# Optimization experiments

Hardware: AMD Instinct MI355X
Metric: run time of the kernel (lower is better)

The kernel has to match this reference:

```python
import jax, jax.numpy as jnp
import numpy as np

ALPHA = 0.2  # LeakyReLU negative slope


def setup_inputs() -> dict:
    key = jax.random.key(0)
    k1, k2, k3, k4 = jax.random.split(key, 4)
    B, T, D_in, H, S = 32, 1024, 64, 64, 2
    embedding = jax.random.normal(k1, (B, T, D_in), dtype=jnp.float32)
    x = jax.random.normal(k2, (S * B, T, D_in), dtype=jnp.float32)
    # xavier_uniform-ish scale for params
    W = jax.random.normal(k3, (D_in, H), dtype=jnp.float32) * (1.414 * np.sqrt(2.0 / (D_in + H)))
    a = jax.random.normal(k4, (2 * H, 1), dtype=jnp.float32) * (1.414 * np.sqrt(2.0 / (2 * H + 1)))
    return {"embedding": embedding, "x": x, "W": W, "a": a, "input_size": S}


def reference(embedding, x, W, a, input_size):
    # embedding: [B, T, D_in], W: [D_in, H], a: [2H, 1], x: [S*B, T, D_in]
    H = W.shape[1]
    h = jnp.einsum("btd,dh->bth", embedding, W)          # [B, T, H]
    a1 = a[:H, 0]                                        # attends to h_i (query side)
    a2 = a[H:, 0]                                        # attends to h_j (key side)
    f1 = h @ a1                                          # [B, T]
    f2 = h @ a2                                          # [B, T]
    # e_ij = leakyrelu(a1.h_i + a2.h_j) -- avoids materializing [B,T,T,2H]
    e = jax.nn.leaky_relu(f1[:, :, None] + f2[:, None, :], negative_slope=ALPHA)  # [B, T, T]
    attn = jax.nn.softmax(e, axis=2)                     # [B, T, T]
    attn_tiled = jnp.tile(attn, (input_size, 1, 1))      # [S*B, T, T] (dropout: eval mode, identity)
    out = jnp.einsum("bij,bjd->bid", attn_tiled, x)      # [S*B, T, D_in]
    return out
```

## Files before the change

kernel.cpp:

```cpp
#include <hip/hip_runtime.h>

typedef float  f32x4 __attribute__((ext_vector_type(4)));
typedef _Float16 h16x8 __attribute__((ext_vector_type(8)));
typedef _Float16 h16x2 __attribute__((ext_vector_type(2)));

#define LOG2E 1.4426950408889634f
#define ALPHA 0.2f

__device__ __forceinline__ float fexp2(float v) {
#if __has_builtin(__builtin_amdgcn_exp2f)
  return __builtin_amdgcn_exp2f(v);
#else
  return exp2f(v);
#endif
}

__global__ __launch_bounds__(256) void fkern(
    const float* __restrict__ emb, const float* __restrict__ W,
    const float* __restrict__ a, float* __restrict__ f1, float* __restrict__ f2)
{
  __shared__ float w1s[64], w2s[64];
  const int t = threadIdx.x;
  if (t < 128) {
    const int d = t & 63;
    const float* wrow = W + d * 64;
    const float* av = a + (t >> 6) * 64;
    float s = 0.f;
#pragma unroll
    for (int h = 0; h < 64; ++h) s = fmaf(wrow[h], av[h], s);
    if (t < 64) w1s[d] = s; else w2s[d] = s;
  }
  __syncthreads();
  const int R = blockIdx.x * 64 + (t >> 2);
  const int q = t & 3;
  const f32x4* er = (const f32x4*)(emb + (size_t)R * 64 + q * 16);
  float s1 = 0.f, s2 = 0.f;
#pragma unroll
  for (int r = 0; r < 4; ++r) {
    f32x4 v = er[r];
#pragma unroll
    for (int c = 0; c < 4; ++c) {
      s1 = fmaf(v[c], w1s[q * 16 + r * 4 + c], s1);
      s2 = fmaf(v[c], w2s[q * 16 + r * 4 + c], s2);
    }
  }
  s1 += __shfl_xor(s1, 1); s1 += __shfl_xor(s1, 2);
  s2 += __shfl_xor(s2, 1); s2 += __shfl_xor(s2, 2);
  if (q == 0) { f1[R] = s1 * LOG2E; f2[R] = s2 * LOG2E; }
}

__global__ __launch_bounds__(512, 1) void attn_main(
    const float* __restrict__ x, const float* __restrict__ f1g,
    const float* __restrict__ f2g, float* __restrict__ out)
{
  __shared__ __attribute__((aligned(16))) _Float16 Xt[2][128 * 136];
  __shared__ float f2s[1024];
  __shared__ float red[4];

  const int t    = threadIdx.x;
  const int wid  = t >> 6;
  const int lane = t & 63;
  const int l15  = lane & 15;
  const int g    = lane >> 4;
  const int wc   = wid & 1;
  const int wr   = wid >> 1;
  const int b    = blockIdx.x >> 3;
  const int brow = (blockIdx.x & 7) * 128;

  if (t < 256) {
    f32x4 v = *(const f32x4*)(f2g + b * 1024 + t * 4);
    *(f32x4*)(f2s + t * 4) = v;
    float m = fmaxf(fmaxf(v[0], v[1]), fmaxf(v[2], v[3]));
#pragma unroll
    for (int off = 1; off < 64; off <<= 1) m = fmaxf(m, __shfl_xor(m, off));
    if (lane == 0) red[wid] = m;
  }

  const float f1v0 = f1g[b * 1024 + brow + wr * 32 + l15];
  const float f1v1 = f1g[b * 1024 + brow + wr * 32 + 16 + l15];

  float rv[32];

  auto stage_loads = [&](int kc) {
#pragma unroll
    for (int p = 0; p < 4; ++p) {
      const int pp = wid * 4 + p;
      const int h  = pp >> 4;
      const int j0 = (pp & 15) * 8;
      const float* base = x + (size_t)(b + 32 * h) * 65536
                            + (size_t)(kc * 128 + j0 + 2 * g) * 64 + l15;
#pragma unroll
      for (int i = 0; i < 4; ++i) {
        rv[p * 8 + i]     = base[i * 16];
        rv[p * 8 + 4 + i] = base[64 + i * 16];
      }
    }
  };
  auto stage_writes = [&](int buf) {
#pragma unroll
    for (int p = 0; p < 4; ++p) {
      const int pp = wid * 4 + p;
      const int h  = pp >> 4;
      const int k  = (pp & 15) * 8 + 2 * g;
#pragma unroll
      for (int i = 0; i < 4; ++i) {
        const int row = h * 64 + l15 + 16 * i;
        h16x2 hp;
        hp[0] = (_Float16)rv[p * 8 + i];
        hp[1] = (_Float16)rv[p * 8 + 4 + i];
        *(unsigned*)&Xt[buf][row * 136 + k] = __builtin_bit_cast(unsigned, hp);
      }
    }
  };

  stage_loads(0);
  __syncthreads();
  const float mf2 = fmaxf(fmaxf(red[0], red[1]), fmaxf(red[2], red[3]));
  float A0, B0, A1, B1;
  { const float u = f1v0 + mf2; const float mL = fmaxf(u, ALPHA * u);
    A0 = f1v0 - mL; B0 = fmaf(ALPHA, f1v0, -mL); }
  { const float u = f1v1 + mf2; const float mL = fmaxf(u, ALPHA * u);
    A1 = f1v1 - mL; B1 = fmaf(ALPHA, f1v1, -mL); }
  stage_writes(0);
  __syncthreads();

  f32x4 acc[2][4] = {};
  f32x4 accz[2] = {};
  h16x8 ones;
#pragma unroll
  for (int i = 0; i < 8; ++i) ones[i] = (_Float16)1.0f;

  for (int kc = 0; kc < 8; ++kc) {
    const int buf = kc & 1;
    if (kc < 7) stage_loads(kc + 1);
#pragma unroll
    for (int ks = 0; ks < 4; ++ks) {
      const int jb = kc * 128 + ks * 32 + g * 8;
      f32x4 f2a = *(const f32x4*)(f2s + jb);
      f32x4 f2b = *(const f32x4*)(f2s + jb + 4);
      float fv[8];
#pragma unroll
      for (int i = 0; i < 4; ++i) { fv[i] = f2a[i]; fv[4 + i] = f2b[i]; }
      h16x8 a0, a1;
#pragma unroll
      for (int jj = 0; jj < 4; ++jj) {
        const float fA = fv[2 * jj], fB = fv[2 * jj + 1];
        float p00 = fexp2(fmaxf(A0 + fA, fmaf(ALPHA, fA, B0)));
        float p01 = fexp2(fmaxf(A0 + fB, fmaf(ALPHA, fB, B0)));
        h16x2 pk0 = __builtin_bit_cast(h16x2, __builtin_amdgcn_cvt_pkrtz(p00, p01));
        a0[2 * jj] = pk0[0]; a0[2 * jj + 1] = pk0[1];
        float p10 = fexp2(fmaxf(A1 + fA, fmaf(ALPHA, fA, B1)));
        float p11 = fexp2(fmaxf(A1 + fB, fmaf(ALPHA, fB, B1)));
        h16x2 pk1 = __builtin_bit_cast(h16x2, __builtin_amdgcn_cvt_pkrtz(p10, p11));
        a1[2 * jj] = pk1[0]; a1[2 * jj + 1] = pk1[1];
      }
#pragma unroll
      for (int nf = 0; nf < 4; ++nf) {
        h16x8 bf = *(const h16x8*)&Xt[buf][(wc * 64 + nf * 16 + l15) * 136 + ks * 32 + g * 8];
        acc[0][nf] = __builtin_amdgcn_mfma_f32_16x16x32_f16(a0, bf, acc[0][nf], 0, 0, 0);
        acc[1][nf] = __builtin_amdgcn_mfma_f32_16x16x32_f16(a1, bf, acc[1][nf], 0, 0, 0);
      }
      accz[0] = __builtin_amdgcn_mfma_f32_16x16x32_f16(a0, ones, accz[0], 0, 0, 0);
      accz[1] = __builtin_amdgcn_mfma_f32_16x16x32_f16(a1, ones, accz[1], 0, 0, 0);
    }
    if (kc < 7) stage_writes(buf ^ 1);
    __syncthreads();
  }

  float rz0[4], rz1[4];
#pragma unroll
  for (int r = 0; r < 4; ++r) {
    rz0[r] = 1.0f / accz[0][r];
    rz1[r] = 1.0f / accz[1][r];
  }
  const int i0 = brow + wr * 32;
#pragma unroll
  for (int nf = 0; nf < 4; ++nf) {
    const int n  = wc * 64 + nf * 16 + l15;
    const int bo = b + ((n >= 64) ? 32 : 0);
    float* op = out + (size_t)bo * 65536 + (n & 63);
#pragma unroll
    for (int r = 0; r < 4; ++r) {
      op[(size_t)(i0 + g * 4 + r) * 64]      = acc[0][nf][r] * rz0[r];
      op[(size_t)(i0 + 16 + g * 4 + r) * 64] = acc[1][nf][r] * rz1[r];
    }
  }
}

extern "C" void kernel_launch(void* const* d_in, const int* in_sizes, int n_in,
                              void* d_out, int out_size, void* d_ws, size_t ws_size,
                              hipStream_t stream) {
  const float* emb = (const float*)d_in[0];
  const float* x   = (const float*)d_in[1];
  const float* W   = (const float*)d_in[2];
  const float* a   = (const float*)d_in[3];
  float* f1 = (float*)d_ws;
  float* f2 = f1 + 32 * 1024;
  fkern<<<512, 256, 0, stream>>>(emb, W, a, f1, f2);
  attn_main<<<256, 512, 0, stream>>>(x, f1, f2, (float*)d_out);
}
```

Baseline: 37.76 us.

## Factor leaky-relu exponent into precomputed exp terms and widen block to 1024 threads

Rewrites exp2(leakyrelu(f1+f2)-m) as a max of two products of per-row and per-column exponentials, precomputing exp2(f2) and exp2(alpha*f2) once per block in shared memory so the inner loop only multiplies and takes a max. The block grows to 1024 threads with each wave owning 16 query rows, and the shared X tile switches from row padding to an XOR swizzle to avoid bank conflicts. This removes the transcendental cost from the inner loop and adds more waves per CU. The trade-off is more LDS traffic per MFMA, and the unshifted exp2(f2) could overflow or lose precision for large logits.

```diff
diff --git a/kernel.cpp b/kernel.cpp
--- a/kernel.cpp
+++ b/kernel.cpp
@@ -49,13 +49,13 @@
   if (q == 0) { f1[R] = s1 * LOG2E; f2[R] = s2 * LOG2E; }
 }
 
-__global__ __launch_bounds__(512, 1) void attn_main(
+__global__ __launch_bounds__(1024, 1) void attn_main(
     const float* __restrict__ x, const float* __restrict__ f1g,
     const float* __restrict__ f2g, float* __restrict__ out)
 {
-  __shared__ __attribute__((aligned(16))) _Float16 Xt[2][128 * 136];
-  __shared__ float f2s[1024];
-  __shared__ float red[4];
+  __shared__ __attribute__((aligned(16))) _Float16 Xt[2][128 * 128];
+  __shared__ float e1s[1024], e2s[1024];
+  __shared__ float red[16];
 
   const int t    = threadIdx.x;
   const int wid  = t >> 6;
@@ -67,24 +67,12 @@
   const int b    = blockIdx.x >> 3;
   const int brow = (blockIdx.x & 7) * 128;
 
-  if (t < 256) {
-    f32x4 v = *(const f32x4*)(f2g + b * 1024 + t * 4);
-    *(f32x4*)(f2s + t * 4) = v;
-    float m = fmaxf(fmaxf(v[0], v[1]), fmaxf(v[2], v[3]));
-#pragma unroll
-    for (int off = 1; off < 64; off <<= 1) m = fmaxf(m, __shfl_xor(m, off));
-    if (lane == 0) red[wid] = m;
-  }
-
-  const float f1v0 = f1g[b * 1024 + brow + wr * 32 + l15];
-  const float f1v1 = f1g[b * 1024 + brow + wr * 32 + 16 + l15];
-
-  float rv[32];
+  float rv[16];
 
   auto stage_loads = [&](int kc) {
 #pragma unroll
-    for (int p = 0; p < 4; ++p) {
-      const int pp = wid * 4 + p;
+    for (int p = 0; p < 2; ++p) {
+      const int pp = wid * 2 + p;
       const int h  = pp >> 4;
       const int j0 = (pp & 15) * 8;
       const float* base = x + (size_t)(b + 32 * h) * 65536
@@ -98,37 +86,52 @@
   };
   auto stage_writes = [&](int buf) {
 #pragma unroll
-    for (int p = 0; p < 4; ++p) {
-      const int pp = wid * 4 + p;
+    for (int p = 0; p < 2; ++p) {
+      const int pp = wid * 2 + p;
       const int h  = pp >> 4;
-      const int k  = (pp & 15) * 8 + 2 * g;
+      const int k8 = pp & 15;
 #pragma unroll
       for (int i = 0; i < 4; ++i) {
         const int row = h * 64 + l15 + 16 * i;
+        const int kb  = k8 ^ (row & 7);
         h16x2 hp;
         hp[0] = (_Float16)rv[p * 8 + i];
         hp[1] = (_Float16)rv[p * 8 + 4 + i];
-        *(unsigned*)&Xt[buf][row * 136 + k] = __builtin_bit_cast(unsigned, hp);
+        *(unsigned*)&Xt[buf][row * 128 + kb * 8 + 2 * g] = __builtin_bit_cast(unsigned, hp);
       }
     }
   };
 
   stage_loads(0);
+
+  {
+    const float v = f2g[b * 1024 + t];
+    e1s[t] = fexp2(v);
+    e2s[t] = fexp2(ALPHA * v);
+    float m = v;
+#pragma unroll
+    for (int off = 1; off < 64; off <<= 1) m = fmaxf(m, __shfl_xor(m, off));
+    if (lane == 0) red[wid] = m;
+  }
+  const float f1v = f1g[b * 1024 + brow + wr * 16 + l15];
   __syncthreads();
-  const float mf2 = fmaxf(fmaxf(red[0], red[1]), fmaxf(red[2], red[3]));
-  float A0, B0, A1, B1;
-  { const float u = f1v0 + mf2; const float mL = fmaxf(u, ALPHA * u);
-    A0 = f1v0 - mL; B0 = fmaf(ALPHA, f1v0, -mL); }
-  { const float u = f1v1 + mf2; const float mL = fmaxf(u, ALPHA * u);
-    A1 = f1v1 - mL; B1 = fmaf(ALPHA, f1v1, -mL); }
+  float mf2 = red[0];
+#pragma unroll
+  for (int i = 1; i < 16; ++i) mf2 = fmaxf(mf2, red[i]);
+  const float u  = f1v + mf2;
+  const float mL = fmaxf(u, ALPHA * u);
+  const float CA = fexp2(f1v - mL);
+  const float CB = fexp2(fmaf(ALPHA, f1v, -mL));
   stage_writes(0);
   __syncthreads();
 
-  f32x4 acc[2][4] = {};
-  f32x4 accz[2] = {};
+  f32x4 acc[4] = {};
+  f32x4 accz = {};
   h16x8 ones;
 #pragma unroll
   for (int i = 0; i < 8; ++i) ones[i] = (_Float16)1.0f;
+
+  const int l7 = l15 & 7;
 
   for (int kc = 0; kc < 8; ++kc) {
     const int buf = kc & 1;
@@ -136,53 +139,49 @@
 #pragma unroll
     for (int ks = 0; ks < 4; ++ks) {
       const int jb = kc * 128 + ks * 32 + g * 8;
-      f32x4 f2a = *(const f32x4*)(f2s + jb);
-      f32x4 f2b = *(const f32x4*)(f2s + jb + 4);
-      float fv[8];
-#pragma unroll
-      for (int i = 0; i < 4; ++i) { fv[i] = f2a[i]; fv[4 + i] = f2b[i]; }
-      h16x8 a0, a1;
+      f32x4 e1a = *(const f32x4*)(e1s + jb);
+      f32x4 e1b = *(const f32x4*)(e1s + jb + 4);
+      f32x4 e2a = *(const f32x4*)(e2s + jb);
+      f32x4 e2b = *(const f32x4*)(e2s + jb + 4);
+      float ev1[8], ev2[8];
+#pragma unroll
+      for (int i = 0; i < 4; ++i) {
+        ev1[i] = e1a[i]; ev1[4 + i] = e1b[i];
+        ev2[i] = e2a[i]; ev2[4 + i] = e2b[i];
+      }
+      h16x8 a0;
 #pragma unroll
       for (int jj = 0; jj < 4; ++jj) {
-        const float fA = fv[2 * jj], fB = fv[2 * jj + 1];
-        float p00 = fexp2(fmaxf(A0 + fA, fmaf(ALPHA, fA, B0)));
-        float p01 = fexp2(fmaxf(A0 + fB, fmaf(ALPHA, fB, B0)));
-        h16x2 pk0 = __builtin_bit_cast(h16x2, __builtin_amdgcn_cvt_pkrtz(p00, p01));
-        a0[2 * jj] = pk0[0]; a0[2 * jj + 1] = pk0[1];
-        float p10 = fexp2(fmaxf(A1 + fA, fmaf(ALPHA, fA, B1)));
-        float p11 = fexp2(fmaxf(A1 + fB, fmaf(ALPHA, fB, B1)));
-        h16x2 pk1 = __builtin_bit_cast(h16x2, __builtin_amdgcn_cvt_pkrtz(p10, p11));
-        a1[2 * jj] = pk1[0]; a1[2 * jj + 1] = pk1[1];
+        float p0 = fmaxf(CA * ev1[2 * jj],     CB * ev2[2 * jj]);
+        float p1 = fmaxf(CA * ev1[2 * jj + 1], CB * ev2[2 * jj + 1]);
+        h16x2 pk = __builtin_bit_cast(h16x2, __builtin_amdgcn_cvt_pkrtz(p0, p1));
+        a0[2 * jj] = pk[0]; a0[2 * jj + 1] = pk[1];
       }
 #pragma unroll
       for (int nf = 0; nf < 4; ++nf) {
-        h16x8 bf = *(const h16x8*)&Xt[buf][(wc * 64 + nf * 16 + l15) * 136 + ks * 32 + g * 8];
-        acc[0][nf] = __builtin_amdgcn_mfma_f32_16x16x32_f16(a0, bf, acc[0][nf], 0, 0, 0);
-        acc[1][nf] = __builtin_amdgcn_mfma_f32_16x16x32_f16(a1, bf, acc[1][nf], 0, 0, 0);
-      }
-      accz[0] = __builtin_amdgcn_mfma_f32_16x16x32_f16(a0, ones, accz[0], 0, 0, 0);
-      accz[1] = __builtin_amdgcn_mfma_f32_16x16x32_f16(a1, ones, accz[1], 0, 0, 0);
+        const int row = wc * 64 + nf * 16 + l15;
+        const int kb  = (ks * 4 + g) ^ l7;
+        h16x8 bf = *(const h16x8*)&Xt[buf][row * 128 + kb * 8];
+        acc[nf] = __builtin_amdgcn_mfma_f32_16x16x32_f16(a0, bf, acc[nf], 0, 0, 0);
+      }
+      accz = __builtin_amdgcn_mfma_f32_16x16x32_f16(a0, ones, accz, 0, 0, 0);
     }
     if (kc < 7) stage_writes(buf ^ 1);
     __syncthreads();
   }
 
-  float rz0[4], rz1[4];
-#pragma unroll
-  for (int r = 0; r < 4; ++r) {
-    rz0[r] = 1.0f / accz[0][r];
-    rz1[r] = 1.0f / accz[1][r];
-  }
-  const int i0 = brow + wr * 32;
+  float rz[4];
+#pragma unroll
+  for (int r = 0; r < 4; ++r) rz[r] = 1.0f / accz[r];
+  const int i0 = brow + wr * 16;
+  const int bo = b + 32 * wc;
+  float* op = out + (size_t)bo * 65536;
 #pragma unroll
   for (int nf = 0; nf < 4; ++nf) {
-    const int n  = wc * 64 + nf * 16 + l15;
-    const int bo = b + ((n >= 64) ? 32 : 0);
-    float* op = out + (size_t)bo * 65536 + (n & 63);
+    const int n = nf * 16 + l15;
 #pragma unroll
     for (int r = 0; r < 4; ++r) {
-      op[(size_t)(i0 + g * 4 + r) * 64]      = acc[0][nf][r] * rz0[r];
-      op[(size_t)(i0 + 16 + g * 4 + r) * 64] = acc[1][nf][r] * rz1[r];
+      op[(size_t)(i0 + g * 4 + r) * 64 + n] = acc[nf][r] * rz[r];
     }
   }
 }
@@ -197,5 +196,5 @@
   float* f1 = (float*)d_ws;
   float* f2 = f1 + 32 * 1024;
   fkern<<<512, 256, 0, stream>>>(emb, W, a, f1, f2);
-  attn_main<<<256, 512, 0, stream>>>(x, f1, f2, (float*)d_out);
-}
+  attn_main<<<256, 1024, 0, stream>>>(x, f1, f2, (float*)d_out);
+}
```

New measurement: 38.34 us. Within noise of the previous version (+1.5%).
